# Optimization experiments

Hardware: AMD Instinct MI355X
Metric: run time of the kernel (lower is better)

## Reference

```python
import jax, jax.numpy as jnp
import numpy as np

NUM_GRAPHS = 16
EPS = 1e-5
HEADS = 4


def setup_inputs() -> dict:
    key = jax.random.key(0)
    ks = jax.random.split(key, 20)
    N, E, D = 100000, 1600000, 128
    s = 1.0 / np.sqrt(D)
    inp = {
        'x': jax.random.normal(ks[0], (N, 6), jnp.float32),
        'edge_index': jax.random.randint(ks[1], (2, E), 0, N),
        'norm': jax.random.uniform(ks[2], (E,), jnp.float32),
        'batch': jnp.sort(jax.random.randint(ks[3], (N,), 0, NUM_GRAPHS)),
        'num_layers': 5,
        'enc_w': jax.random.normal(ks[4], (D, 6), jnp.float32) * 0.4,
        'gru_wih': jax.random.normal(ks[5], (3 * D, D), jnp.float32) * s,
        'gru_whh': jax.random.normal(ks[6], (3 * D, D), jnp.float32) * s,
        'gru_bih': jax.random.normal(ks[7], (3 * D,), jnp.float32) * 0.01,
        'gru_bhh': jax.random.normal(ks[8], (3 * D,), jnp.float32) * 0.01,
        'gn_w': jnp.ones((D,), jnp.float32),
        'gn_b': jnp.zeros((D,), jnp.float32),
        'gn_ms': jnp.ones((D,), jnp.float32),
        'in_proj_w': jax.random.normal(ks[9], (3 * D, D), jnp.float32) * s,
        'in_proj_b': jnp.zeros((3 * D,), jnp.float32),
        'out_w': jax.random.normal(ks[10], (D, D), jnp.float32) * s,
        'out_b': jnp.zeros((D,), jnp.float32),
        'dec1_w': jax.random.normal(ks[11], (D // 2, D), jnp.float32) * s,
        'dec2_w': jax.random.normal(ks[12], (1, D // 2), jnp.float32) * s,
    }
    return inp


def _graph_norm(h, batch, gn_w, gn_b, gn_ms):
    # PyG GraphNorm: per-graph mean/var with learnable mean_scale
    cnt = jax.ops.segment_sum(jnp.ones((h.shape[0], 1), h.dtype), batch,
                              num_segments=NUM_GRAPHS)  # [G,1]
    mean = jax.ops.segment_sum(h, batch, num_segments=NUM_GRAPHS) / cnt  # [G,D]
    out = h - mean[batch] * gn_ms
    var = jax.ops.segment_sum(out * out, batch, num_segments=NUM_GRAPHS) / cnt
    return out * jax.lax.rsqrt(var[batch] + EPS) * gn_w + gn_b


def _gru_cell(xin, h, wih, whh, bih, bhh):
    D = h.shape[-1]
    gi = xin @ wih.T + bih  # [N,3D]
    gh = h @ whh.T + bhh
    r = jax.nn.sigmoid(gi[:, :D] + gh[:, :D])
    z = jax.nn.sigmoid(gi[:, D:2 * D] + gh[:, D:2 * D])
    n = jnp.tanh(gi[:, 2 * D:] + r * gh[:, 2 * D:])
    return (1.0 - z) * n + z * h


def reference(x, edge_index, norm, batch, num_layers, enc_w, gru_wih, gru_whh,
              gru_bih, gru_bhh, gn_w, gn_b, gn_ms, in_proj_w, in_proj_b,
              out_w, out_b, dec1_w, dec2_w):
    N = x.shape[0]
    D = enc_w.shape[0]
    src, dst = edge_index[0], edge_index[1]

    h = jax.nn.leaky_relu(x @ enc_w.T)  # dropout is identity in eval
    h_list = [h]
    prev = h
    for _ in range(num_layers):
        # scatter-add neighborhood aggregation: sum_j norm_e * h[src_e] at dst_e
        agg = jax.ops.segment_sum(norm[:, None] * prev[src], dst, num_segments=N)
        h = _gru_cell(agg, prev, gru_wih, gru_whh, gru_bih, gru_bhh) + prev
        h = _graph_norm(h, batch, gn_w, gn_b, gn_ms)
        h_list.append(h)
        prev = h

    hs = jnp.stack(h_list, axis=1)  # [N, S, D], S = num_layers+1
    S = hs.shape[1]
    dh = D // HEADS
    qkv = hs @ in_proj_w.T + in_proj_b  # [N,S,3D]
    q, k, v = jnp.split(qkv, 3, axis=-1)
    q = q.reshape(N, S, HEADS, dh)
    k = k.reshape(N, S, HEADS, dh)
    v = v.reshape(N, S, HEADS, dh)
    scores = jnp.einsum('nshd,nthd->nhst', q, k) / np.sqrt(dh)
    attn = jax.nn.softmax(scores, axis=-1)  # attn dropout off in eval
    ctx = jnp.einsum('nhst,nthd->nshd', attn, v).reshape(N, S, D)
    h_final = ctx @ out_w.T + out_b + hs
    z = jnp.sum(h_final, axis=1)  # [N,D]

    y = jax.nn.leaky_relu(z @ dec1_w.T)
    y = y @ dec2_w.T  # [N,1]
    return y.reshape(-1)
```

## Files before the change

### kernel.cpp

```cpp
#include <hip/hip_runtime.h>

#define NL 5
#define SS 6
#define DD 128
#define GG 16
#define GNB 16
#define APB 8
#define SCB 1024

typedef __bf16 bf16x8 __attribute__((ext_vector_type(8)));
typedef float f32x4 __attribute__((ext_vector_type(4)));
typedef unsigned short ushort_t;

__device__ __forceinline__ float bf2f(unsigned int u) {
  union { unsigned int i; float f; } c; c.i = u << 16; return c.f;
}
__device__ __forceinline__ unsigned short f2bf(float f) {
  union { float f; unsigned int i; } c; c.f = f;
  unsigned int r = c.i + 0x7FFFu + ((c.i >> 16) & 1u);
  return (unsigned short)(r >> 16);
}

__global__ void k_deg(const int* __restrict__ ei, int E, int* __restrict__ deg) {
  int e = blockIdx.x * 256 + threadIdx.x;
  if (e < E) atomicAdd(&deg[ei[E + e]], 1);
}

__global__ void k_scan1(const int* __restrict__ deg, int* __restrict__ off,
                        int* __restrict__ bsum, int N) {
  __shared__ int tmp[SCB];
  int t = threadIdx.x, i = blockIdx.x * SCB + t;
  int v = (i < N) ? deg[i] : 0;
  tmp[t] = v; __syncthreads();
  for (int o = 1; o < SCB; o <<= 1) {
    int a = (t >= o) ? tmp[t - o] : 0;
    __syncthreads(); tmp[t] += a; __syncthreads();
  }
  if (i < N) off[i] = tmp[t] - v;
  if (t == SCB - 1) bsum[blockIdx.x] = tmp[t];
}

__global__ void k_scan2(int* __restrict__ bsum, int nb) {
  __shared__ int tmp[SCB];
  int t = threadIdx.x;
  int v = (t < nb) ? bsum[t] : 0;
  tmp[t] = v; __syncthreads();
  for (int o = 1; o < SCB; o <<= 1) {
    int a = (t >= o) ? tmp[t - o] : 0;
    __syncthreads(); tmp[t] += a; __syncthreads();
  }
  if (t < nb) bsum[t] = tmp[t] - v;
}

__global__ void k_scan3(int* __restrict__ off, const int* __restrict__ bsum, int N, int E) {
  int i = blockIdx.x * 256 + threadIdx.x;
  if (i < N) off[i] += bsum[i >> 10];
  else if (i == N) off[N] = E;
}

__global__ void k_copy(const int* __restrict__ a, int* __restrict__ b, int n) {
  int i = blockIdx.x * 256 + threadIdx.x;
  if (i < n) b[i] = a[i];
}

__global__ void k_fill(const int* __restrict__ ei, const float* __restrict__ norm, int E,
                       int* __restrict__ cur, int* __restrict__ csrs, float* __restrict__ csrn) {
  int e = blockIdx.x * 256 + threadIdx.x;
  if (e >= E) return;
  int s = ei[e], d = ei[E + e];
  int p = atomicAdd(&cur[d], 1);
  csrs[p] = s;
  csrn[p] = norm[e];
}

__global__ void k_bend(const int* __restrict__ batch, int N, int* __restrict__ endp) {
  int i = blockIdx.x * 256 + threadIdx.x;
  if (i >= N) return;
  int b = batch[i];
  if (i == N - 1 || batch[i + 1] != b) endp[b] = i + 1;
}

__global__ void k_cnt(const int* __restrict__ endp, int* __restrict__ cnt) {
  if (threadIdx.x == 0 && blockIdx.x == 0) {
    int prev = 0;
    for (int g = 0; g < GG; ++g) {
      int e = endp[g];
      if (e > prev) { cnt[g] = e - prev; prev = e; }
      else cnt[g] = 0;
    }
  }
}

__global__ void k_wconv(const float* __restrict__ wih, const float* __restrict__ whh,
                        const float* __restrict__ ipw, const float* __restrict__ ow,
                        const float* __restrict__ d1,
                        ushort_t* __restrict__ WB, ushort_t* __restrict__ WI,
                        ushort_t* __restrict__ WO, ushort_t* __restrict__ WD1) {
  int o = blockIdx.x * 256 + threadIdx.x;
  int seg, idx;
  if (o < 98304) { seg = 0; idx = o; }
  else if (o < 98304 + 49152) { seg = 1; idx = o - 98304; }
  else if (o < 98304 + 49152 + 16384) { seg = 2; idx = o - 98304 - 49152; }
  else if (o < 98304 + 49152 + 16384 + 8192) { seg = 3; idx = o - 98304 - 49152 - 16384; }
  else return;
  int j = idx & 7, l = (idx >> 3) & 63, ks = (idx >> 9) & 3, ctg = idx >> 11;
  int row = ctg * 16 + (l & 15);
  int col = ks * 32 + ((l >> 4) << 3) + j;
  float v;
  if (seg == 0) { v = (row < 384) ? wih[row * 128 + col] : whh[(row - 384) * 128 + col]; WB[idx] = f2bf(v); }
  else if (seg == 1) { WI[idx] = f2bf(ipw[row * 128 + col]); }
  else if (seg == 2) { WO[idx] = f2bf(ow[row * 128 + col]); }
  else { WD1[idx] = f2bf(d1[row * 128 + col]); }
}

__global__ void k_encode(const float* __restrict__ x, const float* __restrict__ ew,
                         ushort_t* __restrict__ HS, int N) {
  int idx = blockIdx.x * 256 + threadIdx.x;
  if (idx >= N * DD) return;
  int n = idx >> 7, d = idx & 127;
  float a = 0.f;
#pragma unroll
  for (int k = 0; k < 6; ++k) a += x[n * 6 + k] * ew[d * 6 + k];
  a = a > 0.f ? a : 0.01f * a;
  HS[((size_t)n * SS) * DD + d] = f2bf(a);
}

__global__ __launch_bounds__(256) void k_agg(const ushort_t* __restrict__ HS, int l,
    const int* __restrict__ off, const int* __restrict__ csrs, const float* __restrict__ csrn,
    ushort_t* __restrict__ AGG, float* __restrict__ SUMS, int N) {
  if (blockIdx.x == 0) {
    for (int i = threadIdx.x; i < 2 * GG * DD; i += 256) SUMS[i] = 0.f;
  }
  int n = blockIdx.x * 4 + (threadIdx.x >> 6);
  if (n >= N) return;
  int lane = threadIdx.x & 63;
  int p0 = off[n], p1 = off[n + 1];
  float ax = 0.f, ay = 0.f;
  const ushort_t* base = HS + l * DD + lane * 2;
  int p = p0;
  for (; p + 8 <= p1; p += 8) {
    int s[8]; float w[8]; unsigned int u[8];
#pragma unroll
    for (int q = 0; q < 8; ++q) { s[q] = csrs[p + q]; w[q] = csrn[p + q]; }
#pragma unroll
    for (int q = 0; q < 8; ++q) u[q] = *(const unsigned int*)(base + (size_t)s[q] * (SS * DD));
#pragma unroll
    for (int q = 0; q < 8; ++q) {
      ax += w[q] * bf2f(u[q] & 0xffffu);
      ay += w[q] * bf2f(u[q] >> 16);
    }
  }
  for (; p < p1; ++p) {
    int s0 = csrs[p];
    float w0 = csrn[p];
    unsigned int u0 = *(const unsigned int*)(base + (size_t)s0 * (SS * DD));
    ax += w0 * bf2f(u0 & 0xffffu);
    ay += w0 * bf2f(u0 >> 16);
  }
  unsigned int pk = (unsigned int)f2bf(ax) | ((unsigned int)f2bf(ay) << 16);
  *(unsigned int*)&AGG[(size_t)n * DD + lane * 2] = pk;
}

__global__ __launch_bounds__(256) void k_gru(const ushort_t* __restrict__ AGG,
    ushort_t* __restrict__ HS, int l,
    const ushort_t* __restrict__ WB,
    const float* __restrict__ bih, const float* __restrict__ bhh,
    const int* __restrict__ batch, float* __restrict__ SUMS, int N) {
  __shared__ ushort_t axh[2][GNB][136];
  __shared__ ushort_t hout[GNB][136];
  float* SUMSQ = SUMS + GG * DD;
  int t = threadIdx.x;
  int nb = blockIdx.x * GNB;
  {
    int n = t >> 4, k8 = (t & 15) << 3;
    int gn = nb + n;
    uint4 xv = make_uint4(0, 0, 0, 0), hv = xv;
    if (gn < N) {
      xv = *(const uint4*)&AGG[(size_t)gn * DD + k8];
      hv = *(const uint4*)&HS[((size_t)gn * SS + l) * DD + k8];
    }
    *(uint4*)&axh[0][n][k8] = xv;
    *(uint4*)&axh[1][n][k8] = hv;
  }
  __syncthreads();
  int w = t >> 6, lane = t & 63, r = lane & 15, kl = lane >> 4;
  bf16x8 afx[4], afh[4];
#pragma unroll
  for (int ks = 0; ks < 4; ++ks) {
    afx[ks] = *(const bf16x8*)&axh[0][r][ks * 32 + kl * 8];
    afh[ks] = *(const bf16x8*)&axh[1][r][ks * 32 + kl * 8];
  }
  f32x4 acc[6][2];
#pragma unroll
  for (int q = 0; q < 6; ++q) {
#pragma unroll
    for (int ct2 = 0; ct2 < 2; ++ct2) {
      int ctg = q * 8 + w * 2 + ct2;
      f32x4 a = {0.f, 0.f, 0.f, 0.f};
#pragma unroll
      for (int ks = 0; ks < 4; ++ks) {
        bf16x8 bf = *(const bf16x8*)&WB[(((size_t)ctg * 4 + ks) << 9) + (lane << 3)];
        a = __builtin_amdgcn_mfma_f32_16x16x32_bf16(q < 3 ? afx[ks] : afh[ks], bf, a, 0, 0, 0);
      }
      acc[q][ct2] = a;
    }
  }
  int nlast = min(nb + GNB, N) - 1;
  int bu = batch[nb];
  bool uni = (batch[nlast] == bu);
#pragma unroll
  for (int ct2 = 0; ct2 < 2; ++ct2) {
    int d = w * 32 + ct2 * 16 + r;
    float br = bih[d], bz = bih[128 + d], bn2 = bih[256 + d];
    float cr = bhh[d], cz = bhh[128 + d], cn2 = bhh[256 + d];
    float loc = 0.f, locq = 0.f;
#pragma unroll
    for (int i = 0; i < 4; ++i) {
      int n = kl * 4 + i;
      int gn = nb + n;
      if (gn < N) {
        float gir = acc[0][ct2][i] + br, giz = acc[1][ct2][i] + bz, gin = acc[2][ct2][i] + bn2;
        float ghr = acc[3][ct2][i] + cr, ghz = acc[4][ct2][i] + cz, ghn = acc[5][ct2][i] + cn2;
        float rr = 1.f / (1.f + __expf(-(gir + ghr)));
        float zz = 1.f / (1.f + __expf(-(giz + ghz)));
        float nn = tanhf(gin + rr * ghn);
        float prev = bf2f(axh[1][n][d]);
        float hp = (1.f - zz) * nn + zz * prev + prev;
        hout[n][d] = f2bf(hp);
        if (uni) { loc += hp; locq += hp * hp; }
        else {
          atomicAdd(&SUMS[batch[gn] * DD + d], hp);
          atomicAdd(&SUMSQ[batch[gn] * DD + d], hp * hp);
        }
      }
    }
    if (uni) {
      loc += __shfl_xor(loc, 16);
      loc += __shfl_xor(loc, 32);
      locq += __shfl_xor(locq, 16);
      locq += __shfl_xor(locq, 32);
      if (kl == 0) {
        atomicAdd(&SUMS[bu * DD + d], loc);
        atomicAdd(&SUMSQ[bu * DD + d], locq);
      }
    }
  }
  __syncthreads();
  {
    int n = t >> 4, k8 = (t & 15) << 3;
    int gn = nb + n;
    if (gn < N)
      *(uint4*)&HS[((size_t)gn * SS + l + 1) * DD + k8] = *(const uint4*)&hout[n][k8];
  }
}

__global__ void k_gn(ushort_t* __restrict__ HS, int slot,
    const float* __restrict__ SUMS, const int* __restrict__ CNT,
    const int* __restrict__ batch, const float* __restrict__ gms,
    const float* __restrict__ gw, const float* __restrict__ gb, int N) {
  const float* SUMSQ = SUMS + GG * DD;
  int idx = blockIdx.x * 256 + threadIdx.x;
  if (idx >= N * 16) return;
  int n = idx >> 4, d0 = (idx & 15) << 3;
  int b = batch[n];
  float inv = 1.f / (float)CNT[b];
  size_t o = ((size_t)n * SS + slot) * DD + d0;
  uint4 hv = *(const uint4*)&HS[o];
  unsigned int uu[4] = {hv.x, hv.y, hv.z, hv.w};
  unsigned int out[4];
#pragma unroll
  for (int j = 0; j < 4; ++j) {
    unsigned short res[2];
#pragma unroll
    for (int k = 0; k < 2; ++k) {
      int d = d0 + j * 2 + k;
      float mean = SUMS[b * DD + d] * inv;
      float m = mean * gms[d];
      float var = SUMSQ[b * DD + d] * inv - 2.f * m * mean + m * m;
      float h = bf2f(k ? (uu[j] >> 16) : (uu[j] & 0xffffu));
      float v = (h - m) * rsqrtf(var + 1e-5f) * gw[d] + gb[d];
      res[k] = f2bf(v);
    }
    out[j] = (unsigned int)res[0] | ((unsigned int)res[1] << 16);
  }
  uint4 ov = make_uint4(out[0], out[1], out[2], out[3]);
  *(uint4*)&HS[o] = ov;
}

__global__ __launch_bounds__(256) void k_attn(const ushort_t* __restrict__ HS,
    const ushort_t* __restrict__ WI, const float* __restrict__ ipb,
    const ushort_t* __restrict__ WO, const float* __restrict__ ob,
    const ushort_t* __restrict__ WD1, const float* __restrict__ d2,
    float* __restrict__ y, int N) {
  __shared__ ushort_t hsb[64][136];
  __shared__ ushort_t qk[4][2][16][40];
  __shared__ ushort_t ctxb[16][136];
  __shared__ float hss[8][132];
  ushort_t (*zb)[136] = (ushort_t(*)[136])&qk[0][0][0][0];
  float* ypart = &hss[0][0];
  int t = threadIdx.x;
  int nb = blockIdx.x * APB;
  for (int idx = t; idx < 64 * 16; idx += 256) {
    int row = idx >> 4, k8 = (idx & 15) << 3;
    int n = row >> 3, s = row & 7;
    uint4 v = make_uint4(0, 0, 0, 0);
    if (s < 6 && nb + n < N) v = *(const uint4*)&HS[((size_t)(nb + n) * SS + s) * DD + k8];
    *(uint4*)&hsb[row][k8] = v;
  }
  __syncthreads();
  {
    int n = t >> 5, d0 = (t & 31) << 2;
    float a0 = 0.f, a1 = 0.f, a2 = 0.f, a3 = 0.f;
#pragma unroll
    for (int s = 0; s < 6; ++s) {
      const ushort_t* rp = &hsb[n * 8 + s][d0];
      unsigned int u0 = *(const unsigned int*)rp;
      unsigned int u1 = *(const unsigned int*)(rp + 2);
      a0 += bf2f(u0 & 0xffffu); a1 += bf2f(u0 >> 16);
      a2 += bf2f(u1 & 0xffffu); a3 += bf2f(u1 >> 16);
    }
    hss[n][d0] = a0; hss[n][d0 + 1] = a1; hss[n][d0 + 2] = a2; hss[n][d0 + 3] = a3;
  }
  int w = t >> 6, lane = t & 63, r = lane & 15, kl = lane >> 4;
  const float sc32 = 0.17677669529663687f;
#pragma unroll
  for (int rt = 0; rt < 4; ++rt) {
    bf16x8 af[4];
#pragma unroll
    for (int ks = 0; ks < 4; ++ks)
      af[ks] = *(const bf16x8*)&hsb[rt * 16 + r][ks * 32 + kl * 8];
    float vreg[2][4];
#pragma unroll
    for (int ct2 = 0; ct2 < 2; ++ct2) {
      int cq = 2 * w + ct2, ck = 8 + 2 * w + ct2, cv = 16 + 2 * w + ct2;
      f32x4 aq = {0.f, 0.f, 0.f, 0.f}, ak = aq, av = aq;
#pragma unroll
      for (int ks = 0; ks < 4; ++ks) {
        bf16x8 bq = *(const bf16x8*)&WI[(((size_t)cq * 4 + ks) << 9) + (lane << 3)];
        bf16x8 bk = *(const bf16x8*)&WI[(((size_t)ck * 4 + ks) << 9) + (lane << 3)];
        bf16x8 bv = *(const bf16x8*)&WI[(((size_t)cv * 4 + ks) << 9) + (lane << 3)];
        aq = __builtin_amdgcn_mfma_f32_16x16x32_bf16(af[ks], bq, aq, 0, 0, 0);
        ak = __builtin_amdgcn_mfma_f32_16x16x32_bf16(af[ks], bk, ak, 0, 0, 0);
        av = __builtin_amdgcn_mfma_f32_16x16x32_bf16(af[ks], bv, av, 0, 0, 0);
      }
      int colh = ct2 * 16 + r;
      float bq = ipb[w * 32 + colh];
      float bk = ipb[128 + w * 32 + colh];
#pragma unroll
      for (int i = 0; i < 4; ++i) {
        qk[w][0][kl * 4 + i][colh] = f2bf((aq[i] + bq) * sc32);
        qk[w][1][kl * 4 + i][colh] = f2bf(ak[i] + bk);
        vreg[ct2][i] = av[i];
      }
    }
    bf16x8 aq = *(const bf16x8*)&qk[w][0][r][kl * 8];
    bf16x8 bk = *(const bf16x8*)&qk[w][1][r][kl * 8];
    f32x4 s4 = {0.f, 0.f, 0.f, 0.f};
    s4 = __builtin_amdgcn_mfma_f32_16x16x32_bf16(aq, bk, s4, 0, 0, 0);
    bool tval = (r & 7) < 6;
    float mx = -1e30f;
    float sc[4]; bool val[4];
#pragma unroll
    for (int i = 0; i < 4; ++i) {
      int s = 4 * kl + i;
      val[i] = tval && (((s ^ r) & 8) == 0) && ((s & 7) < 6);
      sc[i] = s4[i];
      if (val[i]) mx = fmaxf(mx, sc[i]);
    }
#pragma unroll
    for (int m = 1; m <= 4; m <<= 1) mx = fmaxf(mx, __shfl_xor(mx, m));
    float e[4], sum[4];
#pragma unroll
    for (int i = 0; i < 4; ++i) {
      e[i] = val[i] ? __expf(sc[i] - mx) : 0.f;
      sum[i] = e[i];
#pragma unroll
      for (int m = 1; m <= 4; m <<= 1) sum[i] += __shfl_xor(sum[i], m);
    }
    float awp = 0.f;
#pragma unroll
    for (int i = 0; i < 4; ++i) {
      int s = 4 * kl + i;
      float attn = (((s & 7) < 6) && sum[i] > 0.f) ? e[i] / sum[i] : 0.f;
      awp += attn;
    }
    awp += __shfl_xor(awp, 16);
    awp += __shfl_xor(awp, 32);
    float awv[4];
#pragma unroll
    for (int i = 0; i < 4; ++i) {
      int tt = 4 * (kl & 1) + i;
      awv[i] = __shfl(awp, (kl >> 1) * 8 + (tt < 8 ? tt : 0));
    }
    int node = 2 * rt + (kl >> 1);
#pragma unroll
    for (int ct2 = 0; ct2 < 2; ++ct2) {
      float acc = 0.f;
#pragma unroll
      for (int i = 0; i < 4; ++i) {
        int tt = 4 * (kl & 1) + i;
        if (tt < 6) acc += awv[i] * vreg[ct2][i];
      }
      acc += __shfl_xor(acc, 16);
      int dcol = w * 32 + ct2 * 16 + r;
      if ((kl & 1) == 0) ctxb[node][dcol] = f2bf(acc + 6.f * ipb[256 + dcol]);
    }
  }
  __syncthreads();
  {
    bf16x8 ac[4];
#pragma unroll
    for (int ks = 0; ks < 4; ++ks)
      ac[ks] = *(const bf16x8*)&ctxb[r][ks * 32 + kl * 8];
#pragma unroll
    for (int c2 = 0; c2 < 2; ++c2) {
      int ctg = 2 * w + c2;
      f32x4 a = {0.f, 0.f, 0.f, 0.f};
#pragma unroll
      for (int ks = 0; ks < 4; ++ks) {
        bf16x8 bf = *(const bf16x8*)&WO[(((size_t)ctg * 4 + ks) << 9) + (lane << 3)];
        a = __builtin_amdgcn_mfma_f32_16x16x32_bf16(ac[ks], bf, a, 0, 0, 0);
      }
      int col = ctg * 16 + r;
      float obv = 6.f * ob[col];
#pragma unroll
      for (int i = 0; i < 4; ++i) {
        int row = kl * 4 + i;
        float zv = (row < 8) ? (a[i] + obv + hss[row][col]) : 0.f;
        zb[row][col] = f2bf(zv);
      }
    }
  }
  __syncthreads();
  {
    bf16x8 az[4];
#pragma unroll
    for (int ks = 0; ks < 4; ++ks)
      az[ks] = *(const bf16x8*)&zb[r][ks * 32 + kl * 8];
    f32x4 a = {0.f, 0.f, 0.f, 0.f};
#pragma unroll
    for (int ks = 0; ks < 4; ++ks) {
      bf16x8 bf = *(const bf16x8*)&WD1[(((size_t)w * 4 + ks) << 9) + (lane << 3)];
      a = __builtin_amdgcn_mfma_f32_16x16x32_bf16(az[ks], bf, a, 0, 0, 0);
    }
    float dv = d2[w * 16 + r];
    float part[4];
#pragma unroll
    for (int i = 0; i < 4; ++i) {
      float u = a[i];
      u = u > 0.f ? u : 0.01f * u;
      part[i] = u * dv;
    }
#pragma unroll
    for (int m = 1; m <= 8; m <<= 1) {
#pragma unroll
      for (int i = 0; i < 4; ++i) part[i] += __shfl_xor(part[i], m);
    }
    if (r == 0) {
#pragma unroll
      for (int i = 0; i < 4; ++i) {
        int row = kl * 4 + i;
        if (row < 8) ypart[w * 8 + row] = part[i];
      }
    }
  }
  __syncthreads();
  if (t < 8) {
    float v = ypart[t] + ypart[8 + t] + ypart[16 + t] + ypart[24 + t];
    if (nb + t < N) y[nb + t] = v;
  }
}

extern "C" void kernel_launch(void* const* d_in, const int* in_sizes, int n_in,
                              void* d_out, int out_size, void* d_ws, size_t ws_size,
                              hipStream_t stream) {
  const float* x    = (const float*)d_in[0];
  const int*   ei   = (const int*)d_in[1];
  const float* norm = (const float*)d_in[2];
  const int*   batch= (const int*)d_in[3];
  const float* enc_w= (const float*)d_in[5];
  const float* wih  = (const float*)d_in[6];
  const float* whh  = (const float*)d_in[7];
  const float* bih  = (const float*)d_in[8];
  const float* bhh  = (const float*)d_in[9];
  const float* gw   = (const float*)d_in[10];
  const float* gb   = (const float*)d_in[11];
  const float* gms  = (const float*)d_in[12];
  const float* ipw  = (const float*)d_in[13];
  const float* ipb  = (const float*)d_in[14];
  const float* ow   = (const float*)d_in[15];
  const float* ob   = (const float*)d_in[16];
  const float* d1   = (const float*)d_in[17];
  const float* d2   = (const float*)d_in[18];
  float* y = (float*)d_out;
  int N = in_sizes[3];
  int E = in_sizes[2];

  char* p = (char*)d_ws;
  ushort_t* HS  = (ushort_t*)p;  p += (size_t)N * SS * DD * 2;
  ushort_t* AGG = (ushort_t*)p;  p += (size_t)N * DD * 2;
  ushort_t* WB  = (ushort_t*)p;  p += (size_t)98304 * 2;
  ushort_t* WI  = (ushort_t*)p;  p += (size_t)49152 * 2;
  ushort_t* WO  = (ushort_t*)p;  p += (size_t)16384 * 2;
  ushort_t* WD1 = (ushort_t*)p;  p += (size_t)8192 * 2;
  float* SUMS = (float*)p;       p += GG * DD * 4;
  float* SUMSQ= (float*)p;       p += GG * DD * 4;   (void)SUMSQ;
  int*   CNT  = (int*)p;         p += GG * 4;
  int*   ENDP = (int*)p;         p += GG * 4;
  int*   BSUM = (int*)p;         p += SCB * 4;
  int*   OFF  = (int*)p;         p += ((size_t)N + 1) * 4;
  int*   CUR  = (int*)p;         p += (size_t)N * 4;
  int*   CSRS = (int*)p;         p += (size_t)E * 4;
  float* CSRN = (float*)p;

  int nchunk = (N + SCB - 1) / SCB;

  hipMemsetAsync(CUR, 0, (size_t)N * 4, stream);
  hipMemsetAsync(CNT, 0, 2 * GG * 4, stream);
  k_deg<<<(E + 255) / 256, 256, 0, stream>>>(ei, E, CUR);
  k_scan1<<<nchunk, SCB, 0, stream>>>(CUR, OFF, BSUM, N);
  k_scan2<<<1, SCB, 0, stream>>>(BSUM, nchunk);
  k_scan3<<<(N + 256) / 256, 256, 0, stream>>>(OFF, BSUM, N, E);
  k_copy<<<(N + 255) / 256, 256, 0, stream>>>(OFF, CUR, N);
  k_fill<<<(E + 255) / 256, 256, 0, stream>>>(ei, norm, E, CUR, CSRS, CSRN);
  k_bend<<<(N + 255) / 256, 256, 0, stream>>>(batch, N, ENDP);
  k_cnt<<<1, 64, 0, stream>>>(ENDP, CNT);
  k_wconv<<<672, 256, 0, stream>>>(wih, whh, ipw, ow, d1, WB, WI, WO, WD1);
  k_encode<<<(N * DD + 255) / 256, 256, 0, stream>>>(x, enc_w, HS, N);

  for (int l = 0; l < NL; ++l) {
    k_agg<<<(N + 3) / 4, 256, 0, stream>>>(HS, l, OFF, CSRS, CSRN, AGG, SUMS, N);
    k_gru<<<(N + GNB - 1) / GNB, 256, 0, stream>>>(AGG, HS, l, WB, bih, bhh, batch, SUMS, N);
    k_gn<<<(N * 16 + 255) / 256, 256, 0, stream>>>(HS, l + 1, SUMS, CNT, batch, gms, gw, gb, N);
  }
  k_attn<<<(N + APB - 1) / APB, 256, 0, stream>>>(HS, WI, ipb, WO, ob, WD1, d2, y, N);
}
```

Baseline: 1.346 ms.

## Double GRU rows per block, drop attention LDS staging, vectorize encode

Measured after the change: 1.303 ms. 3.2% less time.

```diff
diff --git a/kernel.cpp b/kernel.cpp
--- a/kernel.cpp
+++ b/kernel.cpp
@@ -4,7 +4,7 @@
 #define SS 6
 #define DD 128
 #define GG 16
-#define GNB 16
+#define GNB 32
 #define APB 8
 #define SCB 1024
 
@@ -15,10 +15,9 @@
 __device__ __forceinline__ float bf2f(unsigned int u) {
   union { unsigned int i; float f; } c; c.i = u << 16; return c.f;
 }
-__device__ __forceinline__ unsigned short f2bf(float f) {
-  union { float f; unsigned int i; } c; c.f = f;
-  unsigned int r = c.i + 0x7FFFu + ((c.i >> 16) & 1u);
-  return (unsigned short)(r >> 16);
+__device__ __forceinline__ ushort_t f2bf(float f) {
+  union { __bf16 b; ushort_t u; } c; c.b = (__bf16)f;
+  return c.u;
 }
 
 __global__ void k_deg(const int* __restrict__ ei, int E, int* __restrict__ deg) {
@@ -116,13 +115,21 @@
 __global__ void k_encode(const float* __restrict__ x, const float* __restrict__ ew,
                          ushort_t* __restrict__ HS, int N) {
   int idx = blockIdx.x * 256 + threadIdx.x;
-  if (idx >= N * DD) return;
-  int n = idx >> 7, d = idx & 127;
-  float a = 0.f;
-#pragma unroll
-  for (int k = 0; k < 6; ++k) a += x[n * 6 + k] * ew[d * 6 + k];
-  a = a > 0.f ? a : 0.01f * a;
-  HS[((size_t)n * SS) * DD + d] = f2bf(a);
+  if (idx >= N * 64) return;
+  int n = idx >> 6, d0 = (idx & 63) << 1;
+  float xr[6];
+#pragma unroll
+  for (int k = 0; k < 6; ++k) xr[k] = x[n * 6 + k];
+  float a0 = 0.f, a1 = 0.f;
+#pragma unroll
+  for (int k = 0; k < 6; ++k) {
+    a0 += xr[k] * ew[d0 * 6 + k];
+    a1 += xr[k] * ew[(d0 + 1) * 6 + k];
+  }
+  a0 = a0 > 0.f ? a0 : 0.01f * a0;
+  a1 = a1 > 0.f ? a1 : 0.01f * a1;
+  unsigned int pk = (unsigned int)f2bf(a0) | ((unsigned int)f2bf(a1) << 16);
+  *(unsigned int*)&HS[((size_t)n * SS) * DD + d0] = pk;
 }
 
 __global__ __launch_bounds__(256) void k_agg(const ushort_t* __restrict__ HS, int l,
@@ -171,8 +178,9 @@
   float* SUMSQ = SUMS + GG * DD;
   int t = threadIdx.x;
   int nb = blockIdx.x * GNB;
-  {
-    int n = t >> 4, k8 = (t & 15) << 3;
+#pragma unroll
+  for (int it = 0; it < 2; ++it) {
+    int n = (t >> 4) + it * 16, k8 = (t & 15) << 3;
     int gn = nb + n;
     uint4 xv = make_uint4(0, 0, 0, 0), hv = xv;
     if (gn < N) {
@@ -184,53 +192,59 @@
   }
   __syncthreads();
   int w = t >> 6, lane = t & 63, r = lane & 15, kl = lane >> 4;
-  bf16x8 afx[4], afh[4];
-#pragma unroll
-  for (int ks = 0; ks < 4; ++ks) {
-    afx[ks] = *(const bf16x8*)&axh[0][r][ks * 32 + kl * 8];
-    afh[ks] = *(const bf16x8*)&axh[1][r][ks * 32 + kl * 8];
-  }
-  f32x4 acc[6][2];
-#pragma unroll
-  for (int q = 0; q < 6; ++q) {
-#pragma unroll
-    for (int ct2 = 0; ct2 < 2; ++ct2) {
-      int ctg = q * 8 + w * 2 + ct2;
-      f32x4 a = {0.f, 0.f, 0.f, 0.f};
-#pragma unroll
-      for (int ks = 0; ks < 4; ++ks) {
-        bf16x8 bf = *(const bf16x8*)&WB[(((size_t)ctg * 4 + ks) << 9) + (lane << 3)];
-        a = __builtin_amdgcn_mfma_f32_16x16x32_bf16(q < 3 ? afx[ks] : afh[ks], bf, a, 0, 0, 0);
-      }
-      acc[q][ct2] = a;
-    }
-  }
   int nlast = min(nb + GNB, N) - 1;
   int bu = batch[nb];
   bool uni = (batch[nlast] == bu);
 #pragma unroll
   for (int ct2 = 0; ct2 < 2; ++ct2) {
+    f32x4 acc[6][2];
+#pragma unroll
+    for (int src = 0; src < 2; ++src) {
+      bf16x8 af[2][4];
+#pragma unroll
+      for (int rt = 0; rt < 2; ++rt)
+#pragma unroll
+        for (int ks = 0; ks < 4; ++ks)
+          af[rt][ks] = *(const bf16x8*)&axh[src][rt * 16 + r][ks * 32 + kl * 8];
+#pragma unroll
+      for (int q3 = 0; q3 < 3; ++q3) {
+        int q = src * 3 + q3;
+        int ctg = q * 8 + w * 2 + ct2;
+        f32x4 a0 = {0.f, 0.f, 0.f, 0.f}, a1 = a0;
+#pragma unroll
+        for (int ks = 0; ks < 4; ++ks) {
+          bf16x8 bf = *(const bf16x8*)&WB[(((size_t)ctg * 4 + ks) << 9) + (lane << 3)];
+          a0 = __builtin_amdgcn_mfma_f32_16x16x32_bf16(af[0][ks], bf, a0, 0, 0, 0);
+          a1 = __builtin_amdgcn_mfma_f32_16x16x32_bf16(af[1][ks], bf, a1, 0, 0, 0);
+        }
+        acc[q][0] = a0;
+        acc[q][1] = a1;
+      }
+    }
     int d = w * 32 + ct2 * 16 + r;
     float br = bih[d], bz = bih[128 + d], bn2 = bih[256 + d];
     float cr = bhh[d], cz = bhh[128 + d], cn2 = bhh[256 + d];
     float loc = 0.f, locq = 0.f;
 #pragma unroll
-    for (int i = 0; i < 4; ++i) {
-      int n = kl * 4 + i;
-      int gn = nb + n;
-      if (gn < N) {
-        float gir = acc[0][ct2][i] + br, giz = acc[1][ct2][i] + bz, gin = acc[2][ct2][i] + bn2;
-        float ghr = acc[3][ct2][i] + cr, ghz = acc[4][ct2][i] + cz, ghn = acc[5][ct2][i] + cn2;
-        float rr = 1.f / (1.f + __expf(-(gir + ghr)));
-        float zz = 1.f / (1.f + __expf(-(giz + ghz)));
-        float nn = tanhf(gin + rr * ghn);
-        float prev = bf2f(axh[1][n][d]);
-        float hp = (1.f - zz) * nn + zz * prev + prev;
-        hout[n][d] = f2bf(hp);
-        if (uni) { loc += hp; locq += hp * hp; }
-        else {
-          atomicAdd(&SUMS[batch[gn] * DD + d], hp);
-          atomicAdd(&SUMSQ[batch[gn] * DD + d], hp * hp);
+    for (int rt = 0; rt < 2; ++rt) {
+#pragma unroll
+      for (int i = 0; i < 4; ++i) {
+        int n = rt * 16 + kl * 4 + i;
+        int gn = nb + n;
+        if (gn < N) {
+          float gir = acc[0][rt][i] + br, giz = acc[1][rt][i] + bz, gin = acc[2][rt][i] + bn2;
+          float ghr = acc[3][rt][i] + cr, ghz = acc[4][rt][i] + cz, ghn = acc[5][rt][i] + cn2;
+          float rr = 1.f / (1.f + __expf(-(gir + ghr)));
+          float zz = 1.f / (1.f + __expf(-(giz + ghz)));
+          float nn = tanhf(gin + rr * ghn);
+          float prev = bf2f(axh[1][n][d]);
+          float hp = (1.f - zz) * nn + zz * prev + prev;
+          hout[n][d] = f2bf(hp);
+          if (uni) { loc += hp; locq += hp * hp; }
+          else {
+            atomicAdd(&SUMS[batch[gn] * DD + d], hp);
+            atomicAdd(&SUMSQ[batch[gn] * DD + d], hp * hp);
+          }
         }
       }
     }
@@ -246,8 +260,9 @@
     }
   }
   __syncthreads();
-  {
-    int n = t >> 4, k8 = (t & 15) << 3;
+#pragma unroll
+  for (int it = 0; it < 2; ++it) {
+    int n = (t >> 4) + it * 16, k8 = (t & 15) << 3;
     int gn = nb + n;
     if (gn < N)
       *(uint4*)&HS[((size_t)gn * SS + l + 1) * DD + k8] = *(const uint4*)&hout[n][k8];
@@ -270,7 +285,7 @@
   unsigned int out[4];
 #pragma unroll
   for (int j = 0; j < 4; ++j) {
-    unsigned short res[2];
+    ushort_t res[2];
 #pragma unroll
     for (int k = 0; k < 2; ++k) {
       int d = d0 + j * 2 + k;
@@ -292,7 +307,6 @@
     const ushort_t* __restrict__ WO, const float* __restrict__ ob,
     const ushort_t* __restrict__ WD1, const float* __restrict__ d2,
     float* __restrict__ y, int N) {
-  __shared__ ushort_t hsb[64][136];
   __shared__ ushort_t qk[4][2][16][40];
   __shared__ ushort_t ctxb[16][136];
   __shared__ float hss[8][132];
@@ -300,24 +314,17 @@
   float* ypart = &hss[0][0];
   int t = threadIdx.x;
   int nb = blockIdx.x * APB;
-  for (int idx = t; idx < 64 * 16; idx += 256) {
-    int row = idx >> 4, k8 = (idx & 15) << 3;
-    int n = row >> 3, s = row & 7;
-    uint4 v = make_uint4(0, 0, 0, 0);
-    if (s < 6 && nb + n < N) v = *(const uint4*)&HS[((size_t)(nb + n) * SS + s) * DD + k8];
-    *(uint4*)&hsb[row][k8] = v;
-  }
-  __syncthreads();
   {
     int n = t >> 5, d0 = (t & 31) << 2;
     float a0 = 0.f, a1 = 0.f, a2 = 0.f, a3 = 0.f;
-#pragma unroll
-    for (int s = 0; s < 6; ++s) {
-      const ushort_t* rp = &hsb[n * 8 + s][d0];
-      unsigned int u0 = *(const unsigned int*)rp;
-      unsigned int u1 = *(const unsigned int*)(rp + 2);
-      a0 += bf2f(u0 & 0xffffu); a1 += bf2f(u0 >> 16);
-      a2 += bf2f(u1 & 0xffffu); a3 += bf2f(u1 >> 16);
+    if (nb + n < N) {
+#pragma unroll
+      for (int s = 0; s < 6; ++s) {
+        const ushort_t* rp = &HS[((size_t)(nb + n) * SS + s) * DD + d0];
+        uint2 u = *(const uint2*)rp;
+        a0 += bf2f(u.x & 0xffffu); a1 += bf2f(u.x >> 16);
+        a2 += bf2f(u.y & 0xffffu); a3 += bf2f(u.y >> 16);
+      }
     }
     hss[n][d0] = a0; hss[n][d0 + 1] = a1; hss[n][d0 + 2] = a2; hss[n][d0 + 3] = a3;
   }
@@ -325,10 +332,16 @@
   const float sc32 = 0.17677669529663687f;
 #pragma unroll
   for (int rt = 0; rt < 4; ++rt) {
+    int row = rt * 16 + r;
+    int node = nb + (row >> 3), s = row & 7;
+    bool valid = (s < 6) && (node < N);
+    const ushort_t* abase = HS + ((size_t)node * SS + s) * DD + kl * 8;
     bf16x8 af[4];
 #pragma unroll
-    for (int ks = 0; ks < 4; ++ks)
-      af[ks] = *(const bf16x8*)&hsb[rt * 16 + r][ks * 32 + kl * 8];
+    for (int ks = 0; ks < 4; ++ks) {
+      bf16x8 z8 = {};
+      af[ks] = valid ? *(const bf16x8*)(abase + ks * 32) : z8;
+    }
     float vreg[2][4];
 #pragma unroll
     for (int ct2 = 0; ct2 < 2; ++ct2) {
@@ -362,8 +375,8 @@
     float sc[4]; bool val[4];
 #pragma unroll
     for (int i = 0; i < 4; ++i) {
-      int s = 4 * kl + i;
-      val[i] = tval && (((s ^ r) & 8) == 0) && ((s & 7) < 6);
+      int ss = 4 * kl + i;
+      val[i] = tval && (((ss ^ r) & 8) == 0) && ((ss & 7) < 6);
       sc[i] = s4[i];
       if (val[i]) mx = fmaxf(mx, sc[i]);
     }
@@ -380,8 +393,8 @@
     float awp = 0.f;
 #pragma unroll
     for (int i = 0; i < 4; ++i) {
-      int s = 4 * kl + i;
-      float attn = (((s & 7) < 6) && sum[i] > 0.f) ? e[i] / sum[i] : 0.f;
+      int ss = 4 * kl + i;
+      float attn = (((ss & 7) < 6) && sum[i] > 0.f) ? e[i] / sum[i] : 0.f;
       awp += attn;
     }
     awp += __shfl_xor(awp, 16);
@@ -392,7 +405,7 @@
       int tt = 4 * (kl & 1) + i;
       awv[i] = __shfl(awp, (kl >> 1) * 8 + (tt < 8 ? tt : 0));
     }
-    int node = 2 * rt + (kl >> 1);
+    int nodei = 2 * rt + (kl >> 1);
 #pragma unroll
     for (int ct2 = 0; ct2 < 2; ++ct2) {
       float acc = 0.f;
@@ -403,7 +416,7 @@
       }
       acc += __shfl_xor(acc, 16);
       int dcol = w * 32 + ct2 * 16 + r;
-      if ((kl & 1) == 0) ctxb[node][dcol] = f2bf(acc + 6.f * ipb[256 + dcol]);
+      if ((kl & 1) == 0) ctxb[nodei][dcol] = f2bf(acc + 6.f * ipb[256 + dcol]);
     }
   }
   __syncthreads();
@@ -526,7 +539,7 @@
   k_bend<<<(N + 255) / 256, 256, 0, stream>>>(batch, N, ENDP);
   k_cnt<<<1, 64, 0, stream>>>(ENDP, CNT);
   k_wconv<<<672, 256, 0, stream>>>(wih, whh, ipw, ow, d1, WB, WI, WO, WD1);
-  k_encode<<<(N * DD + 255) / 256, 256, 0, stream>>>(x, enc_w, HS, N);
+  k_encode<<<(N * 64 + 255) / 256, 256, 0, stream>>>(x, enc_w, HS, N);
 
   for (int l = 0; l < NL; ++l) {
     k_agg<<<(N + 3) / 4, 256, 0, stream>>>(HS, l, OFF, CSRS, CSRN, AGG, SUMS, N);
```
